# Kernel optimization log

Measured on AMD Instinct MI355X. Metric: run time of the kernel, lower is better.

## Reference

```python
import jax, jax.numpy as jnp
import numpy as np

NEG_SLOPE = 0.01  # torch F.leaky_relu default

def leaky_relu(z):
    return jnp.where(z >= 0, z, NEG_SLOPE * z)

def setup_inputs() -> dict:
    key = jax.random.key(0)
    k1, k2, k3, k4, k5, k6, k7 = jax.random.split(key, 7)
    n_nodes, d_feat, n_edges, d_edge = 100000, 64, 1000000, 32
    input_dim, hidden_dim = 2 * d_feat + d_edge, 128
    x = jax.random.normal(k1, (n_nodes, d_feat), dtype=jnp.float32)
    edge_index = jax.random.randint(k2, (2, n_edges), 0, n_nodes, dtype=jnp.int64)
    edge_features = jax.random.normal(k3, (n_edges, d_edge), dtype=jnp.float32)
    lim1 = 1.0 / np.sqrt(input_dim)
    W1 = jax.random.uniform(k4, (hidden_dim, input_dim), minval=-lim1, maxval=lim1, dtype=jnp.float32)
    b1 = jax.random.uniform(k5, (hidden_dim,), minval=-lim1, maxval=lim1, dtype=jnp.float32)
    lim2 = 1.0 / np.sqrt(hidden_dim)
    W2 = jax.random.uniform(k6, (1, hidden_dim), minval=-lim2, maxval=lim2, dtype=jnp.float32)
    b2 = jax.random.uniform(k7, (1,), minval=-lim2, maxval=lim2, dtype=jnp.float32)
    return {"x": x, "edge_index": edge_index, "edge_features": edge_features,
            "W1": W1, "b1": b1, "W2": W2, "b2": b2}

def reference(x, edge_index, edge_features, W1, b1, W2, b2):
    origin, destination = edge_index[0], edge_index[1]
    # gather node features per edge and concat: [E, 2*d_feat + d_edge]
    z = jnp.concatenate([x[origin], x[destination], edge_features], axis=1)
    z = leaky_relu(z @ W1.T + b1)   # [E, hidden]
    z = leaky_relu(z @ W2.T + b2)   # [E, 1]
    return z.reshape(-1)
```

## Files before the change

### kernel.cpp

```cpp
#include <hip/hip_runtime.h>
#include <hip/hip_bf16.h>

typedef __attribute__((ext_vector_type(8)))  short          bf16x8;
typedef __attribute__((ext_vector_type(8)))  unsigned short us8;
typedef __attribute__((ext_vector_type(4)))  unsigned short us4;
typedef __attribute__((ext_vector_type(16))) float          f32x16;

static __device__ __forceinline__ unsigned short f2bf(float f) {
    union { float f; unsigned int u; } v; v.f = f;
    unsigned int u = v.u;
    unsigned int r = u + 0x7fffu + ((u >> 16) & 1u);
    return (unsigned short)(r >> 16);
}

static __device__ __forceinline__ bf16x8 pack8(float4 a, float4 b) {
    bf16x8 r;
    r[0] = (short)f2bf(a.x); r[1] = (short)f2bf(a.y);
    r[2] = (short)f2bf(a.z); r[3] = (short)f2bf(a.w);
    r[4] = (short)f2bf(b.x); r[5] = (short)f2bf(b.y);
    r[6] = (short)f2bf(b.z); r[7] = (short)f2bf(b.w);
    return r;
}

__global__ __launch_bounds__(256) void prep_kernel(
    const float* __restrict__ W1, const float* __restrict__ x,
    unsigned short* __restrict__ w1b, unsigned short* __restrict__ xb,
    int nx, int do_x)
{
    if (blockIdx.x == 0) {
        for (int i = threadIdx.x; i < 128 * 160; i += 256)
            w1b[i] = f2bf(W1[i]);
    } else if (do_x) {
        int n4 = nx >> 2;
        int idx = (blockIdx.x - 1) * 256 + threadIdx.x;
        int stride = (gridDim.x - 1) * 256;
        for (int i = idx; i < n4; i += stride) {
            float4 f = ((const float4*)x)[i];
            us4 o = { f2bf(f.x), f2bf(f.y), f2bf(f.z), f2bf(f.w) };
            ((us4*)xb)[i] = o;
        }
    }
}

#define MFMA4(AF, KS)                                                              \
    {                                                                              \
        const int kb_ = (KS) * 16 + kg * 8;                                        \
        acc[0] = __builtin_amdgcn_mfma_f32_32x32x16_bf16(                          \
            (AF), *(const bf16x8*)&W1s[0 * 32 + m][kb_], acc[0], 0, 0, 0);         \
        acc[1] = __builtin_amdgcn_mfma_f32_32x32x16_bf16(                          \
            (AF), *(const bf16x8*)&W1s[1 * 32 + m][kb_], acc[1], 0, 0, 0);         \
        acc[2] = __builtin_amdgcn_mfma_f32_32x32x16_bf16(                          \
            (AF), *(const bf16x8*)&W1s[2 * 32 + m][kb_], acc[2], 0, 0, 0);         \
        acc[3] = __builtin_amdgcn_mfma_f32_32x32x16_bf16(                          \
            (AF), *(const bf16x8*)&W1s[3 * 32 + m][kb_], acc[3], 0, 0, 0);         \
    }

__global__ __launch_bounds__(256) void edge_mlp2(
    const unsigned short* __restrict__ xb,
    const int* __restrict__ ei, const float* __restrict__ ef,
    const unsigned short* __restrict__ w1b,
    const float* __restrict__ b1, const float* __restrict__ w2,
    const float* __restrict__ b2, float* __restrict__ out, int E, int ntiles)
{
    __shared__ unsigned short W1s[128][168];
    __shared__ float b1s[128];
    __shared__ float w2s[128];

    const int tid  = threadIdx.x;
    const int lane = tid & 63;
    const int wv   = tid >> 6;
    const int m    = lane & 31;
    const int kg   = lane >> 5;
    const int laneoff = wv * 32 + m;

    const int t0 = blockIdx.x * 2;
    const int t1 = t0 + 1;

    auto eidx_of = [&](int tt) -> int {
        if (tt >= ntiles) tt = ntiles - 1;
        long e = (long)tt * 128 + laneoff;
        return (int)(e < (long)E ? e : (long)(E - 1));
    };
    const int eA = eidx_of(t0);
    const int eB = eidx_of(t1);

    int oA = ei[eA], dA = ei[(size_t)E + eA];
    int oB = ei[eB], dB = ei[(size_t)E + eB];
    const float4* peA = (const float4*)(ef + (size_t)eA * 32 + kg * 8);
    const float4* peB = (const float4*)(ef + (size_t)eB * 32 + kg * 8);
    float4 efA0 = peA[0], efA1 = peA[1], efA2 = peA[4], efA3 = peA[5];
    float4 efB0 = peB[0], efB1 = peB[1], efB2 = peB[4], efB3 = peB[5];

    {
        int j = tid >> 1, h = tid & 1;
        const unsigned short* src = w1b + j * 160 + h * 80;
        unsigned short* dst = &W1s[j][h * 80];
        #pragma unroll
        for (int i = 0; i < 10; i++)
            *(us8*)(dst + i * 8) = *(const us8*)(src + i * 8);
    }
    if (tid < 128) { b1s[tid] = b1[tid]; w2s[tid] = w2[tid]; }

    const unsigned short* xk = xb + kg * 8;
    bf16x8 xo[4], xd[4];
    {
        const bf16x8* po = (const bf16x8*)(xk + (size_t)oA * 64);
        const bf16x8* pd = (const bf16x8*)(xk + (size_t)dA * 64);
        #pragma unroll
        for (int ks = 0; ks < 4; ks++) { xo[ks] = po[ks * 2]; xd[ks] = pd[ks * 2]; }
    }
    bf16x8 af8 = pack8(efA0, efA1);
    bf16x8 af9 = pack8(efA2, efA3);

    __syncthreads();

    float b1v[4], w2v[4];
    #pragma unroll
    for (int nt = 0; nt < 4; nt++) {
        b1v[nt] = b1s[nt * 32 + m];
        w2v[nt] = w2s[nt * 32 + m];
    }
    const float b2v = b2[0];

    #pragma unroll
    for (int tt = 0; tt < 2; tt++) {
        const int tcur = (tt == 0) ? t0 : t1;

        f32x16 acc[4];
        #pragma unroll
        for (int i = 0; i < 4; i++)
            #pragma unroll
            for (int r = 0; r < 16; r++) acc[i][r] = 0.0f;

        #pragma unroll
        for (int ks = 0; ks < 4; ks++) MFMA4(xo[ks], ks);
        #pragma unroll
        for (int ks = 0; ks < 4; ks++) MFMA4(xd[ks], ks + 4);
        MFMA4(af8, 8);
        MFMA4(af9, 9);

        float s[16];
        #pragma unroll
        for (int r = 0; r < 16; r++) {
            float a = 0.0f;
            #pragma unroll
            for (int nt = 0; nt < 4; nt++) {
                float h = acc[nt][r] + b1v[nt];
                h = fmaxf(h, 0.01f * h);
                a = fmaf(h, w2v[nt], a);
            }
            s[r] = a;
        }

        if (tt == 0) {
            const bf16x8* po = (const bf16x8*)(xk + (size_t)oB * 64);
            const bf16x8* pd = (const bf16x8*)(xk + (size_t)dB * 64);
            #pragma unroll
            for (int ks = 0; ks < 4; ks++) { xo[ks] = po[ks * 2]; xd[ks] = pd[ks * 2]; }
            af8 = pack8(efB0, efB1);
            af9 = pack8(efB2, efB3);
        }

        #pragma unroll
        for (int k = 0; k < 4; k++) {
            const int msk = 1 << k;
            const int bit = (m >> k) & 1;
            #pragma unroll
            for (int j = 0; j < (8 >> k); j++) {
                float a0 = s[2 * j], a1 = s[2 * j + 1];
                float keep = bit ? a1 : a0;
                float send = bit ? a0 : a1;
                s[j] = keep + __shfl_xor(send, msk, 64);
            }
        }
        float tot = s[0] + __shfl_xor(s[0], 16, 64);

        if ((m & 16) == 0) {
            int row = (m & 3) + 4 * kg + 8 * ((m >> 2) & 3);
            long oidx = (long)tcur * 128 + wv * 32 + row;
            if (oidx < (long)E) {
                float v = tot + b2v;
                out[oidx] = fmaxf(v, 0.01f * v);
            }
        }
    }
}

__global__ __launch_bounds__(256) void edge_mlp_fb(
    const float* __restrict__ x,
    const int* __restrict__ ei, const float* __restrict__ ef,
    const unsigned short* __restrict__ w1b,
    const float* __restrict__ b1, const float* __restrict__ w2,
    const float* __restrict__ b2, float* __restrict__ out, int E)
{
    __shared__ unsigned short W1s[128][168];
    __shared__ float b1s[128];
    __shared__ float w2s[128];

    const int t = threadIdx.x;
    {
        int j = t >> 1, h = t & 1;
        const unsigned short* src = w1b + j * 160 + h * 80;
        unsigned short* dst = &W1s[j][h * 80];
        #pragma unroll
        for (int i = 0; i < 10; i++)
            *(us8*)(dst + i * 8) = *(const us8*)(src + i * 8);
    }
    if (t < 128) { b1s[t] = b1[t]; w2s[t] = w2[t]; }
    __syncthreads();

    const int lane = t & 63;
    const int wv   = t >> 6;
    const int m    = lane & 31;
    const int kg   = lane >> 5;
    const float b2v = b2[0];

    long e = (long)blockIdx.x * 128 + wv * 32 + m;
    int eidx = (int)((e < (long)E) ? e : (long)(E - 1));
    int o = ei[eidx];
    int d = ei[(size_t)E + eidx];

    bf16x8 afrag[10];
    {
        const float4* xo = (const float4*)(x + (size_t)o * 64 + kg * 8);
        const float4* xd = (const float4*)(x + (size_t)d * 64 + kg * 8);
        #pragma unroll
        for (int ks = 0; ks < 4; ks++) afrag[ks]     = pack8(xo[ks * 4], xo[ks * 4 + 1]);
        #pragma unroll
        for (int ks = 0; ks < 4; ks++) afrag[4 + ks] = pack8(xd[ks * 4], xd[ks * 4 + 1]);
        const float4* pef = (const float4*)(ef + (size_t)eidx * 32 + kg * 8);
        #pragma unroll
        for (int ks = 0; ks < 2; ks++)
            afrag[8 + ks] = pack8(pef[ks * 4], pef[ks * 4 + 1]);
    }

    f32x16 acc[4];
    #pragma unroll
    for (int i = 0; i < 4; i++)
        #pragma unroll
        for (int r = 0; r < 16; r++) acc[i][r] = 0.0f;

    #pragma unroll
    for (int ks = 0; ks < 10; ks++) {
        MFMA4(afrag[ks], ks);
    }

    float b1v[4], w2v[4];
    #pragma unroll
    for (int nt = 0; nt < 4; nt++) {
        b1v[nt] = b1s[nt * 32 + m];
        w2v[nt] = w2s[nt * 32 + m];
    }
    float s[16];
    #pragma unroll
    for (int r = 0; r < 16; r++) {
        float a = 0.0f;
        #pragma unroll
        for (int nt = 0; nt < 4; nt++) {
            float h = acc[nt][r] + b1v[nt];
            h = fmaxf(h, 0.01f * h);
            a = fmaf(h, w2v[nt], a);
        }
        s[r] = a;
    }
    #pragma unroll
    for (int k = 0; k < 4; k++) {
        const int msk = 1 << k;
        const int bit = (m >> k) & 1;
        #pragma unroll
        for (int j = 0; j < (8 >> k); j++) {
            float a0 = s[2 * j], a1 = s[2 * j + 1];
            float keep = bit ? a1 : a0;
            float send = bit ? a0 : a1;
            s[j] = keep + __shfl_xor(send, msk, 64);
        }
    }
    float tot = s[0] + __shfl_xor(s[0], 16, 64);

    if ((m & 16) == 0) {
        int row = (m & 3) + 4 * kg + 8 * ((m >> 2) & 3);
        long oidx = (long)blockIdx.x * 128 + wv * 32 + row;
        if (oidx < (long)E) {
            float v = tot + b2v;
            out[oidx] = fmaxf(v, 0.01f * v);
        }
    }
}

extern "C" void kernel_launch(void* const* d_in, const int* in_sizes, int n_in,
                              void* d_out, int out_size, void* d_ws, size_t ws_size,
                              hipStream_t stream)
{
    const float* x  = (const float*)d_in[0];
    const int*   ei = (const int*)d_in[1];
    const float* ef = (const float*)d_in[2];
    const float* W1 = (const float*)d_in[3];
    const float* b1 = (const float*)d_in[4];
    const float* w2 = (const float*)d_in[5];
    const float* b2 = (const float*)d_in[6];
    float* out = (float*)d_out;

    const int E  = in_sizes[1] / 2;
    const int nx = in_sizes[0];

    unsigned short* w1b = (unsigned short*)d_ws;
    unsigned short* xb  = (unsigned short*)((char*)d_ws + 65536);
    const bool use_xb = ws_size >= (size_t)65536 + (size_t)nx * 2;

    prep_kernel<<<use_xb ? 2048 : 1, 256, 0, stream>>>(W1, x, w1b, xb, nx, use_xb ? 1 : 0);
    if (use_xb) {
        const int ntiles = (E + 127) / 128;
        const int nblk = (ntiles + 1) / 2;
        edge_mlp2<<<nblk, 256, 0, stream>>>(xb, ei, ef, w1b, b1, w2, b2, out, E, ntiles);
    } else {
        const int nblk = (E + 127) / 128;
        edge_mlp_fb<<<nblk, 256, 0, stream>>>(x, ei, ef, w1b, b1, w2, b2, out, E);
    }
}
```

Measured before the change: 264.5 us.

## Make edge MLP kernel persistent with software-pipelined gathers across tiles

New measurement: 247.0 us. 6.6% less time.

```diff
diff --git a/kernel.cpp b/kernel.cpp
--- a/kernel.cpp
+++ b/kernel.cpp
@@ -14,12 +14,12 @@
 }
 
 static __device__ __forceinline__ bf16x8 pack8(float4 a, float4 b) {
-    bf16x8 r;
-    r[0] = (short)f2bf(a.x); r[1] = (short)f2bf(a.y);
-    r[2] = (short)f2bf(a.z); r[3] = (short)f2bf(a.w);
-    r[4] = (short)f2bf(b.x); r[5] = (short)f2bf(b.y);
-    r[6] = (short)f2bf(b.z); r[7] = (short)f2bf(b.w);
-    return r;
+    union { unsigned int u[4]; bf16x8 v; } r;
+    asm("v_cvt_pk_bf16_f32 %0, %1, %2" : "=v"(r.u[0]) : "v"(a.x), "v"(a.y));
+    asm("v_cvt_pk_bf16_f32 %0, %1, %2" : "=v"(r.u[1]) : "v"(a.z), "v"(a.w));
+    asm("v_cvt_pk_bf16_f32 %0, %1, %2" : "=v"(r.u[2]) : "v"(b.x), "v"(b.y));
+    asm("v_cvt_pk_bf16_f32 %0, %1, %2" : "=v"(r.u[3]) : "v"(b.z), "v"(b.w));
+    return r.v;
 }
 
 __global__ __launch_bounds__(256) void prep_kernel(
@@ -28,8 +28,11 @@
     int nx, int do_x)
 {
     if (blockIdx.x == 0) {
-        for (int i = threadIdx.x; i < 128 * 160; i += 256)
-            w1b[i] = f2bf(W1[i]);
+        for (int i = threadIdx.x; i < 5120; i += 256) {
+            float4 f = ((const float4*)W1)[i];
+            us4 o = { f2bf(f.x), f2bf(f.y), f2bf(f.z), f2bf(f.w) };
+            ((us4*)w1b)[i] = o;
+        }
     } else if (do_x) {
         int n4 = nx >> 2;
         int idx = (blockIdx.x - 1) * 256 + threadIdx.x;
@@ -55,7 +58,7 @@
             (AF), *(const bf16x8*)&W1s[3 * 32 + m][kb_], acc[3], 0, 0, 0);         \
     }
 
-__global__ __launch_bounds__(256) void edge_mlp2(
+__global__ __launch_bounds__(256) void edge_mlp_p(
     const unsigned short* __restrict__ xb,
     const int* __restrict__ ei, const float* __restrict__ ef,
     const unsigned short* __restrict__ w1b,
@@ -63,8 +66,6 @@
     const float* __restrict__ b2, float* __restrict__ out, int E, int ntiles)
 {
     __shared__ unsigned short W1s[128][168];
-    __shared__ float b1s[128];
-    __shared__ float w2s[128];
 
     const int tid  = threadIdx.x;
     const int lane = tid & 63;
@@ -72,116 +73,122 @@
     const int m    = lane & 31;
     const int kg   = lane >> 5;
     const int laneoff = wv * 32 + m;
-
-    const int t0 = blockIdx.x * 2;
-    const int t1 = t0 + 1;
-
-    auto eidx_of = [&](int tt) -> int {
-        if (tt >= ntiles) tt = ntiles - 1;
-        long e = (long)tt * 128 + laneoff;
-        return (int)(e < (long)E ? e : (long)(E - 1));
-    };
-    const int eA = eidx_of(t0);
-    const int eB = eidx_of(t1);
-
-    int oA = ei[eA], dA = ei[(size_t)E + eA];
-    int oB = ei[eB], dB = ei[(size_t)E + eB];
-    const float4* peA = (const float4*)(ef + (size_t)eA * 32 + kg * 8);
-    const float4* peB = (const float4*)(ef + (size_t)eB * 32 + kg * 8);
-    float4 efA0 = peA[0], efA1 = peA[1], efA2 = peA[4], efA3 = peA[5];
-    float4 efB0 = peB[0], efB1 = peB[1], efB2 = peB[4], efB3 = peB[5];
-
+    const int NT = gridDim.x;
+    const int Em1 = E - 1;
+    const int estep = NT * 128;
+
+    int t = blockIdx.x;
+    if (t >= ntiles) return;
+
+    int ecur = min(t * 128 + laneoff, Em1);
+    int o0 = ei[ecur], d0 = ei[(size_t)E + ecur];
     {
-        int j = tid >> 1, h = tid & 1;
-        const unsigned short* src = w1b + j * 160 + h * 80;
-        unsigned short* dst = &W1s[j][h * 80];
-        #pragma unroll
-        for (int i = 0; i < 10; i++)
-            *(us8*)(dst + i * 8) = *(const us8*)(src + i * 8);
-    }
-    if (tid < 128) { b1s[tid] = b1[tid]; w2s[tid] = w2[tid]; }
-
-    const unsigned short* xk = xb + kg * 8;
-    bf16x8 xo[4], xd[4];
-    {
-        const bf16x8* po = (const bf16x8*)(xk + (size_t)oA * 64);
-        const bf16x8* pd = (const bf16x8*)(xk + (size_t)dA * 64);
-        #pragma unroll
-        for (int ks = 0; ks < 4; ks++) { xo[ks] = po[ks * 2]; xd[ks] = pd[ks * 2]; }
-    }
-    bf16x8 af8 = pack8(efA0, efA1);
-    bf16x8 af9 = pack8(efA2, efA3);
-
-    __syncthreads();
-
-    float b1v[4], w2v[4];
-    #pragma unroll
-    for (int nt = 0; nt < 4; nt++) {
-        b1v[nt] = b1s[nt * 32 + m];
-        w2v[nt] = w2s[nt * 32 + m];
-    }
-    const float b2v = b2[0];
-
-    #pragma unroll
-    for (int tt = 0; tt < 2; tt++) {
-        const int tcur = (tt == 0) ? t0 : t1;
-
-        f32x16 acc[4];
-        #pragma unroll
-        for (int i = 0; i < 4; i++)
-            #pragma unroll
-            for (int r = 0; r < 16; r++) acc[i][r] = 0.0f;
-
-        #pragma unroll
-        for (int ks = 0; ks < 4; ks++) MFMA4(xo[ks], ks);
-        #pragma unroll
-        for (int ks = 0; ks < 4; ks++) MFMA4(xd[ks], ks + 4);
-        MFMA4(af8, 8);
-        MFMA4(af9, 9);
-
-        float s[16];
-        #pragma unroll
-        for (int r = 0; r < 16; r++) {
-            float a = 0.0f;
-            #pragma unroll
-            for (int nt = 0; nt < 4; nt++) {
-                float h = acc[nt][r] + b1v[nt];
-                h = fmaxf(h, 0.01f * h);
-                a = fmaf(h, w2v[nt], a);
+        const float4* pe = (const float4*)(ef + (size_t)ecur * 32 + kg * 8);
+        float4 f0 = pe[0], f1 = pe[1], f2 = pe[4], f3 = pe[5];
+        float b1v[4], w2v[4];
+        #pragma unroll
+        for (int nt = 0; nt < 4; nt++) { b1v[nt] = b1[nt * 32 + m]; w2v[nt] = w2[nt * 32 + m]; }
+        const float b2v = b2[0];
+
+        int elin1 = t * 128 + laneoff + estep;
+        int enext = min(elin1, Em1);
+        int o1 = ei[enext], d1 = ei[(size_t)E + enext];
+
+        {
+            int j = tid >> 1, h = tid & 1;
+            const unsigned short* src = w1b + j * 160 + h * 80;
+            unsigned short* dst = &W1s[j][h * 80];
+            #pragma unroll
+            for (int i = 0; i < 10; i++)
+                *(us8*)(dst + i * 8) = *(const us8*)(src + i * 8);
+        }
+
+        const unsigned short* xk = xb + kg * 8;
+        bf16x8 xo[4], xd[4];
+        {
+            const bf16x8* po = (const bf16x8*)(xk + (size_t)o0 * 64);
+            const bf16x8* pd = (const bf16x8*)(xk + (size_t)d0 * 64);
+            #pragma unroll
+            for (int ks = 0; ks < 4; ks++) { xo[ks] = po[ks * 2]; xd[ks] = pd[ks * 2]; }
+        }
+        bf16x8 af8 = pack8(f0, f1);
+        bf16x8 af9 = pack8(f2, f3);
+        {
+            const float4* pe2 = (const float4*)(ef + (size_t)enext * 32 + kg * 8);
+            f0 = pe2[0]; f1 = pe2[1]; f2 = pe2[4]; f3 = pe2[5];
+        }
+
+        __syncthreads();
+
+        while (true) {
+            f32x16 acc[4];
+            #pragma unroll
+            for (int i = 0; i < 4; i++)
+                #pragma unroll
+                for (int r = 0; r < 16; r++) acc[i][r] = 0.0f;
+
+            __builtin_amdgcn_s_setprio(1);
+            #pragma unroll
+            for (int ks = 0; ks < 4; ks++) MFMA4(xo[ks], ks);
+            #pragma unroll
+            for (int ks = 0; ks < 4; ks++) MFMA4(xd[ks], ks + 4);
+            MFMA4(af8, 8);
+            MFMA4(af9, 9);
+            __builtin_amdgcn_s_setprio(0);
+
+            float s[16];
+            #pragma unroll
+            for (int r = 0; r < 16; r++) {
+                float a = 0.0f;
+                #pragma unroll
+                for (int nt = 0; nt < 4; nt++) {
+                    float h = acc[nt][r] + b1v[nt];
+                    h = fmaxf(h, 0.01f * h);
+                    a = fmaf(h, w2v[nt], a);
+                }
+                s[r] = a;
             }
-            s[r] = a;
-        }
-
-        if (tt == 0) {
-            const bf16x8* po = (const bf16x8*)(xk + (size_t)oB * 64);
-            const bf16x8* pd = (const bf16x8*)(xk + (size_t)dB * 64);
-            #pragma unroll
-            for (int ks = 0; ks < 4; ks++) { xo[ks] = po[ks * 2]; xd[ks] = pd[ks * 2]; }
-            af8 = pack8(efB0, efB1);
-            af9 = pack8(efB2, efB3);
-        }
-
-        #pragma unroll
-        for (int k = 0; k < 4; k++) {
-            const int msk = 1 << k;
-            const int bit = (m >> k) & 1;
-            #pragma unroll
-            for (int j = 0; j < (8 >> k); j++) {
-                float a0 = s[2 * j], a1 = s[2 * j + 1];
-                float keep = bit ? a1 : a0;
-                float send = bit ? a0 : a1;
-                s[j] = keep + __shfl_xor(send, msk, 64);
+
+            const int tn = t + NT;
+            const bool more = (tn < ntiles);
+            if (more) {
+                const bf16x8* po = (const bf16x8*)(xk + (size_t)o1 * 64);
+                const bf16x8* pd = (const bf16x8*)(xk + (size_t)d1 * 64);
+                #pragma unroll
+                for (int ks = 0; ks < 4; ks++) { xo[ks] = po[ks * 2]; xd[ks] = pd[ks * 2]; }
+                int e2 = min(elin1 + estep, Em1);
+                o1 = ei[e2]; d1 = ei[(size_t)E + e2];
+                af8 = pack8(f0, f1); af9 = pack8(f2, f3);
+                const float4* pe2 = (const float4*)(ef + (size_t)e2 * 32 + kg * 8);
+                f0 = pe2[0]; f1 = pe2[1]; f2 = pe2[4]; f3 = pe2[5];
             }
-        }
-        float tot = s[0] + __shfl_xor(s[0], 16, 64);
-
-        if ((m & 16) == 0) {
-            int row = (m & 3) + 4 * kg + 8 * ((m >> 2) & 3);
-            long oidx = (long)tcur * 128 + wv * 32 + row;
-            if (oidx < (long)E) {
-                float v = tot + b2v;
-                out[oidx] = fmaxf(v, 0.01f * v);
+
+            #pragma unroll
+            for (int k = 0; k < 4; k++) {
+                const int msk = 1 << k;
+                const int bit = (m >> k) & 1;
+                #pragma unroll
+                for (int j = 0; j < (8 >> k); j++) {
+                    float a0 = s[2 * j], a1 = s[2 * j + 1];
+                    float keep = bit ? a1 : a0;
+                    float send = bit ? a0 : a1;
+                    s[j] = keep + __shfl_xor(send, msk, 64);
+                }
             }
+            float tot = s[0] + __shfl_xor(s[0], 16, 64);
+
+            if ((m & 16) == 0) {
+                int row = (m & 3) + 4 * kg + 8 * ((m >> 2) & 3);
+                long oidx = (long)t * 128 + wv * 32 + row;
+                if (oidx < (long)E) {
+                    float v = tot + b2v;
+                    out[oidx] = fmaxf(v, 0.01f * v);
+                }
+            }
+
+            if (!more) break;
+            t = tn;
+            elin1 += estep;
         }
     }
 }
@@ -310,8 +317,8 @@
     prep_kernel<<<use_xb ? 2048 : 1, 256, 0, stream>>>(W1, x, w1b, xb, nx, use_xb ? 1 : 0);
     if (use_xb) {
         const int ntiles = (E + 127) / 128;
-        const int nblk = (ntiles + 1) / 2;
-        edge_mlp2<<<nblk, 256, 0, stream>>>(xb, ei, ef, w1b, b1, w2, b2, out, E, ntiles);
+        const int nblk = ntiles < 768 ? ntiles : 768;
+        edge_mlp_p<<<nblk, 256, 0, stream>>>(xb, ei, ef, w1b, b1, w2, b2, out, E, ntiles);
     } else {
         const int nblk = (E + 127) / 128;
         edge_mlp_fb<<<nblk, 256, 0, stream>>>(x, ei, ef, w1b, b1, w2, b2, out, E);
```
